# Optimization experiments

Measured on AMD Instinct MI355X. Metric: run time of the kernel, lower is better.

The kernel has to match this reference:

```python
import jax, jax.numpy as jnp
import numpy as np

HIDDEN = 512
IN_FEAT = 512


def setup_inputs() -> dict:
    key = jax.random.key(0)
    ks = jax.random.split(key, 6)
    x = jax.random.normal(ks[0], (128, 1024, IN_FEAT), dtype=jnp.float32)
    # LSTM params: concatenated gates in flax order (i, f, g, o)
    s_in = 1.0 / np.sqrt(IN_FEAT)
    s_h = 1.0 / np.sqrt(HIDDEN)
    Wi = jax.random.normal(ks[1], (IN_FEAT, 4 * HIDDEN), dtype=jnp.float32) * s_in
    Wh = jax.random.normal(ks[2], (HIDDEN, 4 * HIDDEN), dtype=jnp.float32) * s_h
    b = jnp.zeros((4 * HIDDEN,), dtype=jnp.float32)
    Wd = jax.random.normal(ks[3], (HIDDEN, 1), dtype=jnp.float32) * s_h
    bd = jnp.zeros((1,), dtype=jnp.float32)
    return {"x": x, "Wi": Wi, "Wh": Wh, "b": b, "Wd": Wd, "bd": bd}


def reference(x, Wi, Wh, b, Wd, bd):
    B, S, _ = x.shape
    H = Wh.shape[0]
    c0 = jnp.zeros((B, H), dtype=x.dtype)
    h0 = jnp.zeros((B, H), dtype=x.dtype)

    def step(carry, xt):
        c, h = carry
        gates = xt @ Wi + h @ Wh + b  # [B, 4H]
        i, f, g, o = jnp.split(gates, 4, axis=-1)
        c_new = jax.nn.sigmoid(f) * c + jax.nn.sigmoid(i) * jnp.tanh(g)
        h_new = jax.nn.sigmoid(o) * jnp.tanh(c_new)
        return (c_new, h_new), None

    (c_T, h_T), _ = jax.lax.scan(step, (c0, h0), jnp.swapaxes(x, 0, 1))
    # Dense(1) on last timestep output, then squeeze
    return (h_T @ Wd + bd).squeeze(-1)
```

## Files before the change

kernel.cpp:

```cpp
#include <hip/hip_runtime.h>

typedef unsigned int u32;
typedef unsigned short u16;
typedef unsigned long long u64;
typedef float f32x4 __attribute__((ext_vector_type(4)));
typedef _Float16 f16x8 __attribute__((ext_vector_type(8)));

#define S_LEN 1024
#define NG 8
#define NM 32
#define GBAT 16

__device__ __forceinline__ u16 f2h_bits(float f) {
  _Float16 h = (_Float16)f;
  return __builtin_bit_cast(u16, h);
}
__device__ __forceinline__ float h2f_bits(u16 b) {
  return (float)__builtin_bit_cast(_Float16, b);
}
__device__ __forceinline__ u32 pk2(float a, float b) {
  return (u32)f2h_bits(a) | ((u32)f2h_bits(b) << 16);
}
__device__ __forceinline__ u32 pkh(u64 v) {
  return (u32)(v & 0xFFFFu) | (((u32)(v >> 32) & 0xFFFFu) << 16);
}

__global__ __launch_bounds__(256) void prep_frags(const float* __restrict__ Wi,
                                                  const float* __restrict__ Wh,
                                                  uint4* __restrict__ wf4) {
  const int blk = blockIdx.x;
  const int m = blk & 31;
  const float* __restrict__ W = (blk & 32) ? Wh : Wi;
  uint4* __restrict__ dst = wf4 + ((blk & 32) ? 131072 : 0) + m * 4096;
  for (int fi = threadIdx.x; fi < 4096; fi += 256) {
    const int lane = fi & 63;
    const int kc = (fi >> 6) & 15;
    const int q = fi >> 10;
    const int gq = lane >> 4, c = lane & 15;
    const int kb = kc * 32 + gq * 8;
    const int gcol = q * 512 + m * 16 + c;
    u32 wds[4];
#pragma unroll
    for (int pp = 0; pp < 4; ++pp) {
      u16 e0 = f2h_bits(W[(size_t)(kb + 2 * pp) * 2048 + gcol]);
      u16 e1 = f2h_bits(W[(size_t)(kb + 2 * pp + 1) * 2048 + gcol]);
      wds[pp] = (u32)e0 | ((u32)e1 << 16);
    }
    uint4 v; v.x = wds[0]; v.y = wds[1]; v.z = wds[2]; v.w = wds[3];
    dst[fi] = v;
  }
}

__global__ __launch_bounds__(256) void lstm_main(
    const float* __restrict__ x,
    const uint4* __restrict__ wif4,
    u32* __restrict__ hbuf,
    const float* __restrict__ bvec,
    const float* __restrict__ Wd,
    const float* __restrict__ bd,
    float* __restrict__ out) {
  __shared__ __align__(16) uint4 sWi[4096];
  __shared__ __align__(16) uint4 sWh[4096];
  __shared__ float pred[16][256];

  const int tid = threadIdx.x;
  const int lane = tid & 63;
  const int wv = tid >> 6;
  const int g = blockIdx.x & 7;
  const int m = blockIdx.x >> 3;

  {
    for (int i = tid; i < 4096; i += 256) {
      sWi[i] = wif4[m * 4096 + i];
      sWh[i] = wif4[131072 + m * 4096 + i];
    }
  }

  const int bt = tid >> 4;
  const int hi_ = tid & 15;
  const int gb = g * GBAT + bt;
  const int hidx = m * 16 + hi_;

  const float bi = bvec[hidx];
  const float bf_ = bvec[512 + hidx];
  const float bg = bvec[1024 + hidx];
  const float bo = bvec[1536 + hidx];
  float c_reg = 0.f;

  const int abt = lane & 15;
  const int oct = lane >> 4;
  const float* __restrict__ xrow = x + (size_t)(g * GBAT + abt) * (S_LEN * 512);
  const u32 hrow_off = ((u32)(g * GBAT + abt)) << 9;

  __syncthreads();

  for (int t = 0; t < S_LEN; ++t) {
    f32x4 acc0 = {0.f, 0.f, 0.f, 0.f}, acc1 = acc0, acc2 = acc0, acc3 = acc0;

#pragma unroll
    for (int kk = 0; kk < 4; ++kk) {
      const int kc = (wv << 2) | kk;
      const int k0 = kc * 32 + oct * 8;
      const float4* src = reinterpret_cast<const float4*>(xrow + (size_t)t * 512 + k0);
      float4 va = src[0], vb = src[1];
      uint4 av;
      av.x = pk2(va.x, va.y); av.y = pk2(va.z, va.w);
      av.z = pk2(vb.x, vb.y); av.w = pk2(vb.z, vb.w);
      f16x8 af = __builtin_bit_cast(f16x8, av);
      acc0 = __builtin_amdgcn_mfma_f32_16x16x32_f16(af, __builtin_bit_cast(f16x8, sWi[(0 * 16 + kc) * 64 + lane]), acc0, 0, 0, 0);
      acc1 = __builtin_amdgcn_mfma_f32_16x16x32_f16(af, __builtin_bit_cast(f16x8, sWi[(1 * 16 + kc) * 64 + lane]), acc1, 0, 0, 0);
      acc2 = __builtin_amdgcn_mfma_f32_16x16x32_f16(af, __builtin_bit_cast(f16x8, sWi[(2 * 16 + kc) * 64 + lane]), acc2, 0, 0, 0);
      acc3 = __builtin_amdgcn_mfma_f32_16x16x32_f16(af, __builtin_bit_cast(f16x8, sWi[(3 * 16 + kc) * 64 + lane]), acc3, 0, 0, 0);
    }

    if (t > 0) {
      const u64* hp = reinterpret_cast<const u64*>(hbuf + (u32)(t & 1) * 65536u + hrow_off);
      const u32 want = (u32)t;
      const u64 wpat = ((u64)want << 16) | ((u64)want << 48);
      uint4 hv[4];
      for (;;) {
        u64 raw[4][4];
        u64 chk = 0;
#pragma unroll
        for (int kk = 0; kk < 4; ++kk) {
          const int base = (((wv << 2) | kk) << 4) | (oct << 2);
#pragma unroll
          for (int ee = 0; ee < 4; ++ee) {
            raw[kk][ee] = __hip_atomic_load(hp + base + ee, __ATOMIC_RELAXED,
                                            __HIP_MEMORY_SCOPE_AGENT);
            chk |= (raw[kk][ee] ^ wpat) & 0xFFFF0000FFFF0000ull;
          }
        }
        if (__all(chk == 0)) {
#pragma unroll
          for (int kk = 0; kk < 4; ++kk) {
            uint4 t4;
            t4.x = pkh(raw[kk][0]); t4.y = pkh(raw[kk][1]);
            t4.z = pkh(raw[kk][2]); t4.w = pkh(raw[kk][3]);
            hv[kk] = t4;
          }
          break;
        }
        __builtin_amdgcn_s_sleep(1);
      }
#pragma unroll
      for (int kk = 0; kk < 4; ++kk) {
        const int kc = (wv << 2) | kk;
        f16x8 hf = __builtin_bit_cast(f16x8, hv[kk]);
        acc0 = __builtin_amdgcn_mfma_f32_16x16x32_f16(hf, __builtin_bit_cast(f16x8, sWh[(0 * 16 + kc) * 64 + lane]), acc0, 0, 0, 0);
        acc1 = __builtin_amdgcn_mfma_f32_16x16x32_f16(hf, __builtin_bit_cast(f16x8, sWh[(1 * 16 + kc) * 64 + lane]), acc1, 0, 0, 0);
        acc2 = __builtin_amdgcn_mfma_f32_16x16x32_f16(hf, __builtin_bit_cast(f16x8, sWh[(2 * 16 + kc) * 64 + lane]), acc2, 0, 0, 0);
        acc3 = __builtin_amdgcn_mfma_f32_16x16x32_f16(hf, __builtin_bit_cast(f16x8, sWh[(3 * 16 + kc) * 64 + lane]), acc3, 0, 0, 0);
      }
    }

    {
      const int r0 = (lane >> 4) << 2;
      const int cc = lane & 15;
#pragma unroll
      for (int r = 0; r < 4; ++r) {
        pred[wv * 4 + 0][(r0 + r) * 16 + cc] = acc0[r];
        pred[wv * 4 + 1][(r0 + r) * 16 + cc] = acc1[r];
        pred[wv * 4 + 2][(r0 + r) * 16 + cc] = acc2[r];
        pred[wv * 4 + 3][(r0 + r) * 16 + cc] = acc3[r];
      }
    }
    __syncthreads();

    {
      float gi = bi, gf = bf_, gg = bg, go = bo;
#pragma unroll
      for (int w2 = 0; w2 < 4; ++w2) {
        gi += pred[w2 * 4 + 0][tid];
        gf += pred[w2 * 4 + 1][tid];
        gg += pred[w2 * 4 + 2][tid];
        go += pred[w2 * 4 + 3][tid];
      }
      const float si = 1.f / (1.f + __expf(-gi));
      const float sf = 1.f / (1.f + __expf(-gf));
      const float so = 1.f / (1.f + __expf(-go));
      c_reg = sf * c_reg + si * tanhf(gg);
      const float hv_ = so * tanhf(c_reg);
      const u32 word = ((u32)(t + 1) << 16) | (u32)f2h_bits(hv_);
      __hip_atomic_store(hbuf + (u32)((t + 1) & 1) * 65536u + (u32)gb * 512u + (u32)hidx,
                         word, __ATOMIC_RELAXED, __HIP_MEMORY_SCOPE_AGENT);
    }
    __syncthreads();
  }

  if (m == 0) {
    const int btf = tid >> 4;
    const int part = tid & 15;
    const u64* hp = reinterpret_cast<const u64*>(hbuf + (((u32)(g * GBAT + btf)) << 9));
    const u32 want = (u32)S_LEN;
    const u64 wpat = ((u64)want << 16) | ((u64)want << 48);
    float acc = 0.f;
    for (;;) {
      u64 rawv[16];
      u64 chk = 0;
#pragma unroll
      for (int j2 = 0; j2 < 16; ++j2) {
        rawv[j2] = __hip_atomic_load(hp + part * 16 + j2, __ATOMIC_RELAXED,
                                     __HIP_MEMORY_SCOPE_AGENT);
        chk |= (rawv[j2] ^ wpat) & 0xFFFF0000FFFF0000ull;
      }
      if (__all(chk == 0)) {
        acc = 0.f;
#pragma unroll
        for (int j2 = 0; j2 < 16; ++j2) {
          const int k = part * 32 + 2 * j2;
          acc += h2f_bits((u16)(rawv[j2] & 0xFFFFu)) * Wd[k] +
                 h2f_bits((u16)((rawv[j2] >> 32) & 0xFFFFu)) * Wd[k + 1];
        }
        break;
      }
      __builtin_amdgcn_s_sleep(1);
    }
#pragma unroll
    for (int s = 1; s < 16; s <<= 1) acc += __shfl_xor(acc, s, 64);
    if (part == 0) out[g * GBAT + btf] = acc + bd[0];
  }
}

extern "C" void kernel_launch(void* const* d_in, const int* in_sizes, int n_in,
                              void* d_out, int out_size, void* d_ws, size_t ws_size,
                              hipStream_t stream) {
  const float* x = (const float*)d_in[0];
  const float* Wi = (const float*)d_in[1];
  const float* Wh = (const float*)d_in[2];
  const float* bv = (const float*)d_in[3];
  const float* Wd = (const float*)d_in[4];
  const float* bd = (const float*)d_in[5];
  float* out = (float*)d_out;

  char* ws = (char*)d_ws;
  uint4* wif4 = (uint4*)ws;
  u32* hbuf = (u32*)(ws + (4u << 20));

  hipLaunchKernelGGL(prep_frags, dim3(64), dim3(256), 0, stream, Wi, Wh, wif4);

  const float* kx = x;
  const uint4* kw = wif4;
  u32* kh = hbuf;
  const float* kbv = bv;
  const float* kwd = Wd;
  const float* kbd = bd;
  float* ko = out;
  void* args[] = {&kx, &kw, &kh, &kbv, &kwd, &kbd, &ko};
  hipLaunchCooperativeKernel(reinterpret_cast<void*>(lstm_main), dim3(NG * NM),
                             dim3(256), args, 0, stream);
}
```

Measured before the change: 4.342 ms.

## Prefetch next timestep x into registers and vectorize padded gate staging

New measurement: 4.405 ms. About the same (+1.4%).

```diff
diff --git a/kernel.cpp b/kernel.cpp
--- a/kernel.cpp
+++ b/kernel.cpp
@@ -10,6 +10,7 @@
 #define NG 8
 #define NM 32
 #define GBAT 16
+#define PSTR 20
 
 __device__ __forceinline__ u16 f2h_bits(float f) {
   _Float16 h = (_Float16)f;
@@ -61,7 +62,7 @@
     float* __restrict__ out) {
   __shared__ __align__(16) uint4 sWi[4096];
   __shared__ __align__(16) uint4 sWh[4096];
-  __shared__ float pred[16][256];
+  __shared__ __align__(16) float pred[16][PSTR * 16];
 
   const int tid = threadIdx.x;
   const int lane = tid & 63;
@@ -69,11 +70,9 @@
   const int g = blockIdx.x & 7;
   const int m = blockIdx.x >> 3;
 
-  {
-    for (int i = tid; i < 4096; i += 256) {
-      sWi[i] = wif4[m * 4096 + i];
-      sWh[i] = wif4[131072 + m * 4096 + i];
-    }
+  for (int i = tid; i < 4096; i += 256) {
+    sWi[i] = wif4[m * 4096 + i];
+    sWh[i] = wif4[131072 + m * 4096 + i];
   }
 
   const int bt = tid >> 4;
@@ -94,18 +93,35 @@
 
   __syncthreads();
 
-  for (int t = 0; t < S_LEN; ++t) {
+  float4 xa[8], xb[8];
+#pragma unroll
+  for (int kk = 0; kk < 4; ++kk) {
+    const int k0 = ((wv << 2) | kk) * 32 + oct * 8;
+    xa[2 * kk]     = *reinterpret_cast<const float4*>(xrow + k0);
+    xa[2 * kk + 1] = *reinterpret_cast<const float4*>(xrow + k0 + 4);
+  }
+
+  auto step = [&](int t, float4* cur, float4* nxt) {
+    {
+      int tn = t + 1; tn = (tn < S_LEN) ? tn : (S_LEN - 1);
+      const float* xr = xrow + (size_t)tn * 512;
+#pragma unroll
+      for (int kk = 0; kk < 4; ++kk) {
+        const int k0 = ((wv << 2) | kk) * 32 + oct * 8;
+        nxt[2 * kk]     = *reinterpret_cast<const float4*>(xr + k0);
+        nxt[2 * kk + 1] = *reinterpret_cast<const float4*>(xr + k0 + 4);
+      }
+    }
+
     f32x4 acc0 = {0.f, 0.f, 0.f, 0.f}, acc1 = acc0, acc2 = acc0, acc3 = acc0;
-
 #pragma unroll
     for (int kk = 0; kk < 4; ++kk) {
       const int kc = (wv << 2) | kk;
-      const int k0 = kc * 32 + oct * 8;
-      const float4* src = reinterpret_cast<const float4*>(xrow + (size_t)t * 512 + k0);
-      float4 va = src[0], vb = src[1];
       uint4 av;
-      av.x = pk2(va.x, va.y); av.y = pk2(va.z, va.w);
-      av.z = pk2(vb.x, vb.y); av.w = pk2(vb.z, vb.w);
+      av.x = pk2(cur[2 * kk].x, cur[2 * kk].y);
+      av.y = pk2(cur[2 * kk].z, cur[2 * kk].w);
+      av.z = pk2(cur[2 * kk + 1].x, cur[2 * kk + 1].y);
+      av.w = pk2(cur[2 * kk + 1].z, cur[2 * kk + 1].w);
       f16x8 af = __builtin_bit_cast(f16x8, av);
       acc0 = __builtin_amdgcn_mfma_f32_16x16x32_f16(af, __builtin_bit_cast(f16x8, sWi[(0 * 16 + kc) * 64 + lane]), acc0, 0, 0, 0);
       acc1 = __builtin_amdgcn_mfma_f32_16x16x32_f16(af, __builtin_bit_cast(f16x8, sWi[(1 * 16 + kc) * 64 + lane]), acc1, 0, 0, 0);
@@ -155,26 +171,25 @@
     }
 
     {
+      const int cc = lane & 15;
       const int r0 = (lane >> 4) << 2;
-      const int cc = lane & 15;
-#pragma unroll
-      for (int r = 0; r < 4; ++r) {
-        pred[wv * 4 + 0][(r0 + r) * 16 + cc] = acc0[r];
-        pred[wv * 4 + 1][(r0 + r) * 16 + cc] = acc1[r];
-        pred[wv * 4 + 2][(r0 + r) * 16 + cc] = acc2[r];
-        pred[wv * 4 + 3][(r0 + r) * 16 + cc] = acc3[r];
-      }
-    }
-    __syncthreads();
+      *reinterpret_cast<f32x4*>(&pred[wv * 4 + 0][PSTR * cc + r0]) = acc0;
+      *reinterpret_cast<f32x4*>(&pred[wv * 4 + 1][PSTR * cc + r0]) = acc1;
+      *reinterpret_cast<f32x4*>(&pred[wv * 4 + 2][PSTR * cc + r0]) = acc2;
+      *reinterpret_cast<f32x4*>(&pred[wv * 4 + 3][PSTR * cc + r0]) = acc3;
+    }
+    asm volatile("s_waitcnt lgkmcnt(0)" ::: "memory");
+    __builtin_amdgcn_s_barrier();
+    __builtin_amdgcn_sched_barrier(0);
 
     {
       float gi = bi, gf = bf_, gg = bg, go = bo;
 #pragma unroll
       for (int w2 = 0; w2 < 4; ++w2) {
-        gi += pred[w2 * 4 + 0][tid];
-        gf += pred[w2 * 4 + 1][tid];
-        gg += pred[w2 * 4 + 2][tid];
-        go += pred[w2 * 4 + 3][tid];
+        gi += pred[w2 * 4 + 0][PSTR * hi_ + bt];
+        gf += pred[w2 * 4 + 1][PSTR * hi_ + bt];
+        gg += pred[w2 * 4 + 2][PSTR * hi_ + bt];
+        go += pred[w2 * 4 + 3][PSTR * hi_ + bt];
       }
       const float si = 1.f / (1.f + __expf(-gi));
       const float sf = 1.f / (1.f + __expf(-gf));
@@ -185,7 +200,13 @@
       __hip_atomic_store(hbuf + (u32)((t + 1) & 1) * 65536u + (u32)gb * 512u + (u32)hidx,
                          word, __ATOMIC_RELAXED, __HIP_MEMORY_SCOPE_AGENT);
     }
-    __syncthreads();
+    __builtin_amdgcn_s_barrier();
+    __builtin_amdgcn_sched_barrier(0);
+  };
+
+  for (int t = 0; t < S_LEN; t += 2) {
+    step(t, xa, xb);
+    step(t + 1, xb, xa);
   }
 
   if (m == 0) {
```
